# Kernel optimization log

Measured on AMD Instinct MI355X. Metric: run time of the kernel, lower is better.

The kernel has to match this reference:

```python
import jax, jax.numpy as jnp
import numpy as np

# ---- config (from init_kwargs) ----
BASE_SIZE = 16
RATIOS = np.array([0.5, 1.0, 2.0])
N_LAYERS = 3
SCALES = 2.0 ** np.arange(N_LAYERS)
STRIDE = 16
PRE_NMS_TOPN = 2000
POST_NMS_TOPN = 300
MIN_THRESHOLD = 16.0
NMS_THRESH = 0.7
IMG_W = 1024
IMG_H = 1024
B, H, W = 16, 64, 64
A = len(RATIOS) * len(SCALES)  # 9


def _whctrs(a):
    w = a[2] - a[0] + 1.0
    h = a[3] - a[1] + 1.0
    return w, h, a[0] + 0.5 * (w - 1.0), a[1] + 0.5 * (h - 1.0)


def _mkanchors(ws, hs, cx, cy):
    return np.stack([cx - 0.5 * (ws - 1.0), cy - 0.5 * (hs - 1.0),
                     cx + 0.5 * (ws - 1.0), cy + 0.5 * (hs - 1.0)], axis=1)


def _generate_anchors():
    base = np.array([0.0, 0.0, BASE_SIZE - 1.0, BASE_SIZE - 1.0])
    w, h, cx, cy = _whctrs(base)
    size = w * h
    ws = np.round(np.sqrt(size / RATIOS))
    hs = np.round(ws * RATIOS)
    ratio_anchors = _mkanchors(ws, hs, np.full_like(ws, cx), np.full_like(ws, cy))
    out = []
    for ra in ratio_anchors:
        rw, rh, rcx, rcy = _whctrs(ra)
        out.append(_mkanchors(rw * SCALES, rh * SCALES,
                              np.full_like(SCALES, rcx), np.full_like(SCALES, rcy)))
    return np.concatenate(out, axis=0)  # (A, 4)


def _all_anchors(height, width):
    anchors = _generate_anchors()  # (A, 4)
    sx = np.arange(width) * STRIDE
    sy = np.arange(height) * STRIDE
    sx, sy = np.meshgrid(sx, sy)  # (H, W) row-major over y -> matches permute(0,2,3,1)
    shifts = np.stack([sx.ravel(), sy.ravel(), sx.ravel(), sy.ravel()], axis=1)  # (K, 4)
    return (anchors[None, :, :] + shifts[:, None, :]).reshape(-1, 4).astype(np.float32)  # (K*A, 4)


def _decode(deltas, anchors):
    # bbox_reg_to_coord: standard bbox_transform_inv
    aw = anchors[:, 2] - anchors[:, 0] + 1.0
    ah = anchors[:, 3] - anchors[:, 1] + 1.0
    acx = anchors[:, 0] + 0.5 * aw
    acy = anchors[:, 1] + 0.5 * ah
    cx = deltas[..., 0] * aw + acx
    cy = deltas[..., 1] * ah + acy
    pw = jnp.exp(deltas[..., 2]) * aw
    ph = jnp.exp(deltas[..., 3]) * ah
    return jnp.stack([cx - 0.5 * pw, cy - 0.5 * ph,
                      cx + 0.5 * pw, cy + 0.5 * ph], axis=-1)


def _nms_single(boxes, scores):
    # boxes: (N, 4) sorted by descending score
    N = boxes.shape[0]
    x1, y1, x2, y2 = boxes[:, 0], boxes[:, 1], boxes[:, 2], boxes[:, 3]
    areas = (x2 - x1 + 1.0) * (y2 - y1 + 1.0)
    iw = jnp.maximum(0.0, jnp.minimum(x2[:, None], x2[None, :]) - jnp.maximum(x1[:, None], x1[None, :]) + 1.0)
    ih = jnp.maximum(0.0, jnp.minimum(y2[:, None], y2[None, :]) - jnp.maximum(y1[:, None], y1[None, :]) + 1.0)
    inter = iw * ih
    iou = inter / (areas[:, None] + areas[None, :] - inter)  # (N, N)
    idx = jnp.arange(N)

    def body(sup, i):  # greedy sequential NMS
        keep_i = ~sup[i]
        sup = sup | (keep_i & (iou[i] > NMS_THRESH) & (idx > i))
        return sup, keep_i

    _, keep = jax.lax.scan(body, jnp.zeros(N, dtype=bool), idx)
    # kept boxes first, preserving score order; fixed-size output padded with zeros
    prio = jnp.where(keep, idx, idx + N)
    order = jnp.argsort(prio)[:POST_NMS_TOPN]
    valid = keep[order]
    out_boxes = jnp.where(valid[:, None], boxes[order], 0.0)
    out_scores = jnp.where(valid, scores[order], 0.0)
    return out_boxes, out_scores


def reference(labels_pred, bbox_reg):
    b, _, h, w = labels_pred.shape
    anchors = jnp.asarray(_all_anchors(h, w))  # (K*A, 4)
    scores = labels_pred.transpose(0, 2, 3, 1).reshape(b, -1, 2)[..., 1]  # (B, K*A)
    deltas = bbox_reg.transpose(0, 2, 3, 1).reshape(b, -1, 4)  # (B, K*A, 4)
    boxes = _decode(deltas, anchors)
    boxes = jnp.stack([
        jnp.clip(boxes[..., 0], 0.0, IMG_W - 1.0),
        jnp.clip(boxes[..., 1], 0.0, IMG_H - 1.0),
        jnp.clip(boxes[..., 2], 0.0, IMG_W - 1.0),
        jnp.clip(boxes[..., 3], 0.0, IMG_H - 1.0)], axis=-1)
    keep = ((boxes[..., 2] - boxes[..., 0] + 1.0 >= MIN_THRESHOLD)
            & (boxes[..., 3] - boxes[..., 1] + 1.0 >= MIN_THRESHOLD))
    masked = jnp.where(keep, scores, -jnp.inf)
    top_scores, top_idx = jax.lax.top_k(masked, PRE_NMS_TOPN)  # (B, pre)
    top_boxes = jnp.take_along_axis(boxes, top_idx[..., None], axis=1)  # (B, pre, 4)
    return jax.vmap(_nms_single)(top_boxes, top_scores)


def setup_inputs() -> dict:
    key = jax.random.key(0)
    k1, k2 = jax.random.split(key)
    labels_pred = jax.random.normal(k1, (B, 2 * A, H, W), dtype=jnp.float32)
    bbox_reg = jax.random.normal(k2, (B, 4 * A, H, W), dtype=jnp.float32) * 0.2
    return {"labels_pred": labels_pred, "bbox_reg": bbox_reg}
```

## Files before the change

### kernel.cpp

```cpp
#include <hip/hip_runtime.h>
#include <stdint.h>

#pragma clang fp contract(off)

typedef unsigned long long ull;

#define NB 16
#define NA 9
#define HW 4096
#define NANCH (NA*HW)
#define TOTAL (NB*NANCH)
#define TOPN 2000
#define PADN 2048
#define SELPAD 3072
#define OUTN 300
#define HBITS 13
#define HBINS (1 << HBITS)
#define MNMS 384
#define MSTRIPS (MNMS/64)
#define MPITCH 8
#define GD2 16

#define MIDC 0x1.666667p-1

__constant__ float c_ax1[9] = {-3.5f,-15.f,-38.f,  0.f, -8.f,-24.f,  2.5f, -3.f,-14.f};
__constant__ float c_ay1[9] = { 2.f,  -4.f,-16.f,  0.f, -8.f,-24.f, -3.f,-14.f,-36.f};
__constant__ float c_ax2[9] = {18.5f, 30.f, 53.f, 15.f, 23.f, 39.f, 12.5f, 18.f, 29.f};
__constant__ float c_ay2[9] = {13.f,  19.f, 31.f, 15.f, 23.f, 39.f, 18.f,  29.f, 51.f};

__device__ __forceinline__ void decode_box(int a, int x, int y,
    float d0, float d1, float d2, float d3,
    float& x1, float& y1, float& x2, float& y2) {
  float ax1 = c_ax1[a] + 16.f * (float)x;
  float ay1 = c_ay1[a] + 16.f * (float)y;
  float ax2 = c_ax2[a] + 16.f * (float)x;
  float ay2 = c_ay2[a] + 16.f * (float)y;
  float aw  = ax2 - ax1 + 1.f;
  float ah  = ay2 - ay1 + 1.f;
  float acx = ax1 + 0.5f * aw;
  float acy = ay1 + 0.5f * ah;
  float cx = d0 * aw + acx;
  float cy = d1 * ah + acy;
  float pw = expf(d2) * aw;
  float ph = expf(d3) * ah;
  x1 = cx - 0.5f * pw;
  y1 = cy - 0.5f * ph;
  x2 = cx + 0.5f * pw;
  y2 = cy + 0.5f * ph;
  x1 = fminf(fmaxf(x1, 0.f), 1023.f);
  y1 = fminf(fmaxf(y1, 0.f), 1023.f);
  x2 = fminf(fmaxf(x2, 0.f), 1023.f);
  y2 = fminf(fmaxf(y2, 0.f), 1023.f);
}

__device__ __forceinline__ uint32_t f2ord(float f) {
  uint32_t u = __float_as_uint(f);
  return (u & 0x80000000u) ? ~u : (u | 0x80000000u);
}
__device__ __forceinline__ float ord2f(uint32_t u) {
  return (u & 0x80000000u) ? __uint_as_float(u ^ 0x80000000u) : __uint_as_float(~u);
}

__global__ void k_score(const float* __restrict__ labels, const float* __restrict__ bbox,
                        uint32_t* __restrict__ keys) {
  int t = blockIdx.x * 256 + threadIdx.x;
  if (t >= TOTAL) return;
  int pos = t & (HW - 1);
  int ba  = t >> 12;
  int a = ba % 9, b = ba / 9;
  float score = labels[((b * 18 + 2 * a + 1) << 12) + pos];
  const float* dp = bbox + ((b * 36 + 4 * a) << 12) + pos;
  float d0 = dp[0], d1 = dp[4096], d2 = dp[8192], d3 = dp[12288];
  int y = pos >> 6, x = pos & 63;
  float x1, y1, x2, y2;
  decode_box(a, x, y, d0, d1, d2, d3, x1, y1, x2, y2);
  bool keep = (x2 - x1 + 1.f >= 16.f) && (y2 - y1 + 1.f >= 16.f);
  float s = keep ? score : -INFINITY;
  keys[t] = f2ord(s);
}

__global__ __launch_bounds__(1024) void k_batch(const uint32_t* __restrict__ keys,
                                                ull* __restrict__ selKeys,
                                                uint32_t* __restrict__ counters) {
  int b = blockIdx.x, tid = threadIdx.x;
  int wave = tid >> 6, lane = tid & 63;
  __shared__ uint32_t hist[HBINS];
  __shared__ uint32_t wtot[16];
  __shared__ uint32_t sh_T, sh_cnt;
  const uint32_t* kb = keys + b * NANCH;
  const uint4* kb4 = (const uint4*)kb;
#pragma unroll
  for (int k = 0; k < HBINS / 1024; ++k) hist[k * 1024 + tid] = 0u;
  if (tid == 0) { sh_T = 0u; sh_cnt = 0u; }
  __syncthreads();
  for (int i4 = tid; i4 < NANCH / 4; i4 += 1024) {
    uint4 v = kb4[i4];
    if (v.x & 0x80000000u) atomicAdd(&hist[v.x >> (32 - HBITS)], 1u);
    if (v.y & 0x80000000u) atomicAdd(&hist[v.y >> (32 - HBITS)], 1u);
    if (v.z & 0x80000000u) atomicAdd(&hist[v.z >> (32 - HBITS)], 1u);
    if (v.w & 0x80000000u) atomicAdd(&hist[v.w >> (32 - HBITS)], 1u);
  }
  __syncthreads();
  uint32_t c[8], suf[8];
#pragma unroll
  for (int k = 0; k < 8; ++k) c[k] = hist[tid * 8 + k];
  suf[7] = c[7];
#pragma unroll
  for (int k = 6; k >= 0; --k) suf[k] = c[k] + suf[k + 1];
  uint32_t total = suf[0];
  uint32_t wsuf = total;
#pragma unroll
  for (int off = 1; off < 64; off <<= 1) {
    uint32_t v = __shfl_down(wsuf, off);
    if (lane + off < 64) wsuf += v;
  }
  if (lane == 0) wtot[wave] = wsuf;
  __syncthreads();
  uint32_t wab = 0;
  for (int w = wave + 1; w < 16; ++w) wab += wtot[w];
  uint32_t ssum = wsuf + wab;
  uint32_t above_t = ssum - total;
  if (above_t < TOPN && ssum >= TOPN) {
    uint32_t T = (uint32_t)(tid * 8);
#pragma unroll
    for (int k = 7; k >= 0; --k) {
      uint32_t ab = above_t + ((k < 7) ? suf[k + 1] : 0u);
      if (ab < TOPN && ab + c[k] >= TOPN) T = (uint32_t)(tid * 8 + k);
    }
    sh_T = T;
  }
  __syncthreads();
  uint32_t T = sh_T;
  for (int i4 = tid; i4 < NANCH / 4; i4 += 1024) {
    uint4 v = kb4[i4];
    uint32_t vv[4] = { v.x, v.y, v.z, v.w };
#pragma unroll
    for (int cc = 0; cc < 4; ++cc) {
      uint32_t u = vv[cc];
      if ((u >> (32 - HBITS)) >= T) {
        uint32_t slot = atomicAdd(&sh_cnt, 1u);
        if (slot < SELPAD) {
          int i = i4 * 4 + cc;
          uint32_t canon = (uint32_t)((i & 4095) * 9 + (i >> 12));
          selKeys[b * SELPAD + slot] = (((ull)(~u)) << 32) | canon;
        }
      }
    }
  }
  __syncthreads();
  if (tid == 0) counters[b] = (sh_cnt < SELPAD) ? sh_cnt : SELPAD;
}

__global__ __launch_bounds__(256) void k_rank(const ull* __restrict__ selKeys,
                        const uint32_t* __restrict__ counters, const float* __restrict__ bbox,
                        float4* __restrict__ boxes, float* __restrict__ areas,
                        float* __restrict__ selScore) {
  int b = blockIdx.y;
  int i = blockIdx.x * 256 + threadIdx.x;
  int tid = threadIdx.x;
  uint32_t n = counters[b];
  const ull* sk = selKeys + b * SELPAD;
  ull ki = (i < (int)n) ? sk[i] : ~0ull;
  int rank = 0;
  __shared__ ull chunk[256];
  for (uint32_t base = 0; base < n; base += 256) {
    uint32_t j = base + (uint32_t)tid;
    chunk[tid] = (j < n) ? sk[j] : ~0ull;
    __syncthreads();
    int lim = (int)(n - base < 256u ? n - base : 256u);
    for (int t2 = 0; t2 < lim; ++t2) rank += (chunk[t2] < ki) ? 1 : 0;
    __syncthreads();
  }
  if (i < (int)n && rank < TOPN) {
    uint32_t idx = (uint32_t)ki;
    selScore[b * TOPN + rank] = ord2f(~((uint32_t)(ki >> 32)));
    int pos = (int)idx / 9, a = (int)idx - 9 * pos;
    int y = pos >> 6, x = pos & 63;
    const float* dp = bbox + ((b * 36 + 4 * a) << 12) + pos;
    float d0 = dp[0], d1 = dp[4096], d2 = dp[8192], d3 = dp[12288];
    float x1, y1, x2, y2;
    decode_box(a, x, y, d0, d1, d2, d3, x1, y1, x2, y2);
    boxes[b * PADN + rank] = make_float4(x1, y1, x2, y2);
    areas[b * PADN + rank] = (x2 - x1 + 1.f) * (y2 - y1 + 1.f);
  }
}

__global__ __launch_bounds__(256) void k_mask(const float4* __restrict__ boxes,
                                              const float* __restrict__ areas,
                                              ull* __restrict__ gmask) {
  int rb = blockIdx.x, b = blockIdx.y;
  int tid = threadIdx.x, wv = tid >> 6, lane = tid & 63;
  int rbase = rb * 32;
  int smin = rbase >> 6;
  __shared__ float4 sRow[32];
  __shared__ float  sAr[32];
  if (tid < 32) {
    sRow[tid] = boxes[b * PADN + rbase + tid];
    sAr[tid]  = areas[b * PADN + rbase + tid];
  }
  float4 bj[MSTRIPS];
  float  ja[MSTRIPS];
#pragma unroll
  for (int s = 0; s < MSTRIPS; ++s) {
    if (s >= smin) {
      bj[s] = boxes[b * PADN + (s << 6) + lane];
      ja[s] = areas[b * PADN + (s << 6) + lane];
    }
  }
  __syncthreads();
  const double MD = MIDC;
  for (int r = wv; r < 32; r += 4) {
    int i = rbase + r;
    float4 bi = sRow[r];
    float  ia = sAr[r];
#pragma unroll
    for (int s = 0; s < MSTRIPS; ++s) {
      if (s < smin) continue;
      int j = (s << 6) + lane;
      float iw = fminf(bi.z, bj[s].z) - fmaxf(bi.x, bj[s].x) + 1.f; iw = fmaxf(iw, 0.f);
      float ih = fminf(bi.w, bj[s].w) - fmaxf(bi.y, bj[s].y) + 1.f; ih = fmaxf(ih, 0.f);
      float inter = iw * ih;
      float uu = (ia + ja[s]) - inter;
      bool sup = (j > i) && ((double)inter >= MD * (double)uu);
      ull mb = __ballot(sup);
      if (lane == 0) gmask[((size_t)b * MNMS + i) * MPITCH + s] = mb;
    }
  }
}

__global__ __launch_bounds__(64) void k_scan(const ull* __restrict__ gmask,
                                             const float4* __restrict__ boxes,
                                             const float* __restrict__ areas,
                                             const float* __restrict__ selScore,
                                             float* __restrict__ out) {
  int b = blockIdx.x, lane = threadIdx.x;
  const ull* mb = gmask + (size_t)b * MNMS * MPITCH;
  int l8 = lane & 7;
  __shared__ int kidx[OUTN];
  __shared__ int sh_cnt;
  const double MD = MIDC;
  ull supw = 0ull;
  int cnt = 0;
  ull pf[GD2];
#pragma unroll
  for (int ph = 0; ph < GD2; ++ph) pf[ph] = mb[ph * MPITCH + l8];
  for (int base = 0; base < MNMS && cnt < OUTN; base += GD2) {
#pragma unroll
    for (int ph = 0; ph < GD2; ++ph) {
      int i = base + ph;
      ull bal = __ballot(((supw >> (i & 63)) & 1ull) != 0ull);
      if (!((bal >> (i >> 6)) & 1ull)) {
        ull mm = (l8 >= (i >> 6) && l8 < MSTRIPS) ? pf[ph] : 0ull;
        supw |= mm;
        if (lane == 0 && cnt < OUTN) kidx[cnt] = i;
        cnt++;
      }
      int nx = i + GD2; if (nx > MNMS - 1) nx = MNMS - 1;
      pf[ph] = mb[nx * MPITCH + l8];
    }
  }
  for (int i = MNMS; i < TOPN && cnt < OUTN; ++i) {
    float4 bi = boxes[b * PADN + i];
    float ia = areas[b * PADN + i];
    bool sup = false;
    for (int cb = 0; cb < cnt; cb += 64) {
      int k = cb + lane;
      if (k < cnt) {
        int kj = kidx[k];
        float4 bk = boxes[b * PADN + kj];
        float ka = areas[b * PADN + kj];
        float iw = fminf(bi.z, bk.z) - fmaxf(bi.x, bk.x) + 1.f; iw = fmaxf(iw, 0.f);
        float ih = fminf(bi.w, bk.w) - fmaxf(bi.y, bk.y) + 1.f; ih = fmaxf(ih, 0.f);
        float inter = iw * ih;
        float uu = (ia + ka) - inter;
        sup = sup || ((double)inter >= MD * (double)uu);
      }
    }
    if (!__any(sup)) {
      if (lane == 0) kidx[cnt] = i;
      cnt++;
    }
  }
  if (lane == 0) sh_cnt = (cnt < OUTN) ? cnt : OUTN;
  __syncthreads();
  int c = sh_cnt;
  float4* ob = (float4*)out;
  for (int s2 = lane; s2 < OUTN; s2 += 64) {
    float4 bx = make_float4(0.f, 0.f, 0.f, 0.f);
    float sc = 0.f;
    if (s2 < c) {
      int i = kidx[s2];
      bx = boxes[b * PADN + i];
      sc = selScore[b * TOPN + i];
    }
    ob[b * OUTN + s2] = bx;
    out[NB * OUTN * 4 + b * OUTN + s2] = sc;
  }
}

extern "C" void kernel_launch(void* const* d_in, const int* in_sizes, int n_in,
                              void* d_out, int out_size, void* d_ws, size_t ws_size,
                              hipStream_t stream) {
  const float* labels = (const float*)d_in[0];
  const float* bbox   = (const float*)d_in[1];
  char* ws = (char*)d_ws;
  uint32_t* keys    = (uint32_t*)(ws + 0);
  ull* selKeys      = (ull*)(ws + 2359296);
  float* selScore   = (float*)(ws + 2752512);
  float* areas      = (float*)(ws + 2880512);
  float4* boxes     = (float4*)(ws + 3011584);
  uint32_t* counters= (uint32_t*)(ws + 3535872);
  ull* gmask        = (ull*)(ws + 3535936);
  float* out = (float*)d_out;

  hipLaunchKernelGGL(k_score, dim3((TOTAL + 255) / 256), dim3(256), 0, stream, labels, bbox, keys);
  hipLaunchKernelGGL(k_batch, dim3(NB), dim3(1024), 0, stream, keys, selKeys, counters);
  hipLaunchKernelGGL(k_rank,  dim3(SELPAD / 256, NB), dim3(256), 0, stream, selKeys, counters, bbox, boxes, areas, selScore);
  hipLaunchKernelGGL(k_mask,  dim3(MNMS / 32, NB), dim3(256), 0, stream, boxes, areas, gmask);
  hipLaunchKernelGGL(k_scan,  dim3(NB), dim3(64), 0, stream, gmask, boxes, areas, selScore, out);
}
```

Measured before the change: 90.42 us.

## Fuse rank, mask and scan kernels with per-batch atomic flags; vectorize scoring

Merges the rank, IoU-mask and greedy-scan kernels into one launch. Blocks are split by role, and later-stage blocks spin on per-batch global counters that the earlier-stage blocks increment after a threadfence. This removes two kernel launch gaps and lets batches proceed independently. It also vectorizes k_score to handle four anchors per thread with float4 loads and a uint4 store. The spin-wait relies on producer blocks being scheduled before or alongside consumers, which carries a deadlock risk if they are not. The done counters are reset inside k_score.

```diff
diff --git a/kernel.cpp b/kernel.cpp
--- a/kernel.cpp
+++ b/kernel.cpp
@@ -62,21 +62,35 @@
 }
 
 __global__ void k_score(const float* __restrict__ labels, const float* __restrict__ bbox,
-                        uint32_t* __restrict__ keys) {
-  int t = blockIdx.x * 256 + threadIdx.x;
-  if (t >= TOTAL) return;
-  int pos = t & (HW - 1);
-  int ba  = t >> 12;
+                        uint32_t* __restrict__ keys, uint32_t* __restrict__ done) {
+  int t4 = blockIdx.x * 256 + threadIdx.x;
+  if (blockIdx.x == 0) { done[threadIdx.x] = 0u; done[256 + threadIdx.x] = 0u; }
+  int p4 = t4 & 1023;
+  int pos = p4 << 2;
+  int ba = t4 >> 10;
   int a = ba % 9, b = ba / 9;
-  float score = labels[((b * 18 + 2 * a + 1) << 12) + pos];
-  const float* dp = bbox + ((b * 36 + 4 * a) << 12) + pos;
-  float d0 = dp[0], d1 = dp[4096], d2 = dp[8192], d3 = dp[12288];
-  int y = pos >> 6, x = pos & 63;
-  float x1, y1, x2, y2;
-  decode_box(a, x, y, d0, d1, d2, d3, x1, y1, x2, y2);
-  bool keep = (x2 - x1 + 1.f >= 16.f) && (y2 - y1 + 1.f >= 16.f);
-  float s = keep ? score : -INFINITY;
-  keys[t] = f2ord(s);
+  float4 sc  = ((const float4*)(labels + ((b * 18 + 2 * a + 1) << 12)))[p4];
+  const float* dpb = bbox + ((b * 36 + 4 * a) << 12);
+  float4 d0v = ((const float4*)(dpb        ))[p4];
+  float4 d1v = ((const float4*)(dpb +  4096))[p4];
+  float4 d2v = ((const float4*)(dpb +  8192))[p4];
+  float4 d3v = ((const float4*)(dpb + 12288))[p4];
+  int y = pos >> 6, x0 = pos & 63;
+  float scA[4] = { sc.x,  sc.y,  sc.z,  sc.w  };
+  float d0A[4] = { d0v.x, d0v.y, d0v.z, d0v.w };
+  float d1A[4] = { d1v.x, d1v.y, d1v.z, d1v.w };
+  float d2A[4] = { d2v.x, d2v.y, d2v.z, d2v.w };
+  float d3A[4] = { d3v.x, d3v.y, d3v.z, d3v.w };
+  uint32_t kout[4];
+#pragma unroll
+  for (int k = 0; k < 4; ++k) {
+    float x1, y1, x2, y2;
+    decode_box(a, x0 + k, y, d0A[k], d1A[k], d2A[k], d3A[k], x1, y1, x2, y2);
+    bool keep = (x2 - x1 + 1.f >= 16.f) && (y2 - y1 + 1.f >= 16.f);
+    kout[k] = f2ord(keep ? scA[k] : -INFINITY);
+  }
+  ((uint4*)(keys + b * NANCH + (a << 12) + pos))[0] =
+      make_uint4(kout[0], kout[1], kout[2], kout[3]);
 }
 
 __global__ __launch_bounds__(1024) void k_batch(const uint32_t* __restrict__ keys,
@@ -151,150 +165,162 @@
   if (tid == 0) counters[b] = (sh_cnt < SELPAD) ? sh_cnt : SELPAD;
 }
 
-__global__ __launch_bounds__(256) void k_rank(const ull* __restrict__ selKeys,
-                        const uint32_t* __restrict__ counters, const float* __restrict__ bbox,
-                        float4* __restrict__ boxes, float* __restrict__ areas,
-                        float* __restrict__ selScore) {
-  int b = blockIdx.y;
-  int i = blockIdx.x * 256 + threadIdx.x;
-  int tid = threadIdx.x;
-  uint32_t n = counters[b];
-  const ull* sk = selKeys + b * SELPAD;
-  ull ki = (i < (int)n) ? sk[i] : ~0ull;
-  int rank = 0;
-  __shared__ ull chunk[256];
-  for (uint32_t base = 0; base < n; base += 256) {
-    uint32_t j = base + (uint32_t)tid;
-    chunk[tid] = (j < n) ? sk[j] : ~0ull;
-    __syncthreads();
-    int lim = (int)(n - base < 256u ? n - base : 256u);
-    for (int t2 = 0; t2 < lim; ++t2) rank += (chunk[t2] < ki) ? 1 : 0;
-    __syncthreads();
-  }
-  if (i < (int)n && rank < TOPN) {
-    uint32_t idx = (uint32_t)ki;
-    selScore[b * TOPN + rank] = ord2f(~((uint32_t)(ki >> 32)));
-    int pos = (int)idx / 9, a = (int)idx - 9 * pos;
-    int y = pos >> 6, x = pos & 63;
-    const float* dp = bbox + ((b * 36 + 4 * a) << 12) + pos;
-    float d0 = dp[0], d1 = dp[4096], d2 = dp[8192], d3 = dp[12288];
-    float x1, y1, x2, y2;
-    decode_box(a, x, y, d0, d1, d2, d3, x1, y1, x2, y2);
-    boxes[b * PADN + rank] = make_float4(x1, y1, x2, y2);
-    areas[b * PADN + rank] = (x2 - x1 + 1.f) * (y2 - y1 + 1.f);
-  }
-}
-
-__global__ __launch_bounds__(256) void k_mask(const float4* __restrict__ boxes,
-                                              const float* __restrict__ areas,
-                                              ull* __restrict__ gmask) {
-  int rb = blockIdx.x, b = blockIdx.y;
-  int tid = threadIdx.x, wv = tid >> 6, lane = tid & 63;
-  int rbase = rb * 32;
-  int smin = rbase >> 6;
-  __shared__ float4 sRow[32];
-  __shared__ float  sAr[32];
-  if (tid < 32) {
-    sRow[tid] = boxes[b * PADN + rbase + tid];
-    sAr[tid]  = areas[b * PADN + rbase + tid];
-  }
-  float4 bj[MSTRIPS];
-  float  ja[MSTRIPS];
-#pragma unroll
-  for (int s = 0; s < MSTRIPS; ++s) {
-    if (s >= smin) {
-      bj[s] = boxes[b * PADN + (s << 6) + lane];
-      ja[s] = areas[b * PADN + (s << 6) + lane];
-    }
-  }
-  __syncthreads();
+__global__ __launch_bounds__(256) void k_post(
+    const ull* __restrict__ selKeys, const uint32_t* __restrict__ counters,
+    const float* __restrict__ bbox, float4* __restrict__ boxes,
+    float* __restrict__ areas, float* __restrict__ selScore,
+    ull* __restrict__ gmask, float* __restrict__ out, uint32_t* __restrict__ done) {
+  int unit = blockIdx.x, b = blockIdx.y, tid = threadIdx.x;
   const double MD = MIDC;
-  for (int r = wv; r < 32; r += 4) {
-    int i = rbase + r;
-    float4 bi = sRow[r];
-    float  ia = sAr[r];
+
+  if (unit < 12) {
+    int i = unit * 256 + tid;
+    uint32_t n = counters[b];
+    const ull* sk = selKeys + b * SELPAD;
+    ull ki = (i < (int)n) ? sk[i] : ~0ull;
+    int rank = 0;
+    __shared__ ull chunk[256];
+    for (uint32_t base = 0; base < n; base += 256) {
+      uint32_t j = base + (uint32_t)tid;
+      chunk[tid] = (j < n) ? sk[j] : ~0ull;
+      __syncthreads();
+      int lim = (int)(n - base < 256u ? n - base : 256u);
+      for (int t2 = 0; t2 < lim; ++t2) rank += (chunk[t2] < ki) ? 1 : 0;
+      __syncthreads();
+    }
+    if (i < (int)n && rank < TOPN) {
+      uint32_t idx = (uint32_t)ki;
+      selScore[b * TOPN + rank] = ord2f(~((uint32_t)(ki >> 32)));
+      int pos = (int)idx / 9, a = (int)idx - 9 * pos;
+      int y = pos >> 6, x = pos & 63;
+      const float* dp = bbox + ((b * 36 + 4 * a) << 12) + pos;
+      float d0 = dp[0], d1 = dp[4096], d2 = dp[8192], d3 = dp[12288];
+      float x1, y1, x2, y2;
+      decode_box(a, x, y, d0, d1, d2, d3, x1, y1, x2, y2);
+      boxes[b * PADN + rank] = make_float4(x1, y1, x2, y2);
+      areas[b * PADN + rank] = (x2 - x1 + 1.f) * (y2 - y1 + 1.f);
+    }
+    __threadfence();
+    __syncthreads();
+    if (tid == 0) atomicAdd(&done[b * 16], 1u);
+
+  } else if (unit < 24) {
+    if (tid == 0) {
+      while (atomicAdd(&done[b * 16], 0u) < 12u) __builtin_amdgcn_s_sleep(2);
+    }
+    __syncthreads();
+    __threadfence();
+    int rb = unit - 12;
+    int wv = tid >> 6, lane = tid & 63;
+    int rbase = rb * 32;
+    int smin = rbase >> 6;
+    __shared__ float4 sRow[32];
+    __shared__ float  sAr[32];
+    if (tid < 32) {
+      sRow[tid] = boxes[b * PADN + rbase + tid];
+      sAr[tid]  = areas[b * PADN + rbase + tid];
+    }
+    float4 bj[MSTRIPS];
+    float  ja[MSTRIPS];
 #pragma unroll
     for (int s = 0; s < MSTRIPS; ++s) {
-      if (s < smin) continue;
-      int j = (s << 6) + lane;
-      float iw = fminf(bi.z, bj[s].z) - fmaxf(bi.x, bj[s].x) + 1.f; iw = fmaxf(iw, 0.f);
-      float ih = fminf(bi.w, bj[s].w) - fmaxf(bi.y, bj[s].y) + 1.f; ih = fmaxf(ih, 0.f);
-      float inter = iw * ih;
-      float uu = (ia + ja[s]) - inter;
-      bool sup = (j > i) && ((double)inter >= MD * (double)uu);
-      ull mb = __ballot(sup);
-      if (lane == 0) gmask[((size_t)b * MNMS + i) * MPITCH + s] = mb;
-    }
-  }
-}
-
-__global__ __launch_bounds__(64) void k_scan(const ull* __restrict__ gmask,
-                                             const float4* __restrict__ boxes,
-                                             const float* __restrict__ areas,
-                                             const float* __restrict__ selScore,
-                                             float* __restrict__ out) {
-  int b = blockIdx.x, lane = threadIdx.x;
-  const ull* mb = gmask + (size_t)b * MNMS * MPITCH;
-  int l8 = lane & 7;
-  __shared__ int kidx[OUTN];
-  __shared__ int sh_cnt;
-  const double MD = MIDC;
-  ull supw = 0ull;
-  int cnt = 0;
-  ull pf[GD2];
-#pragma unroll
-  for (int ph = 0; ph < GD2; ++ph) pf[ph] = mb[ph * MPITCH + l8];
-  for (int base = 0; base < MNMS && cnt < OUTN; base += GD2) {
-#pragma unroll
-    for (int ph = 0; ph < GD2; ++ph) {
-      int i = base + ph;
-      ull bal = __ballot(((supw >> (i & 63)) & 1ull) != 0ull);
-      if (!((bal >> (i >> 6)) & 1ull)) {
-        ull mm = (l8 >= (i >> 6) && l8 < MSTRIPS) ? pf[ph] : 0ull;
-        supw |= mm;
-        if (lane == 0 && cnt < OUTN) kidx[cnt] = i;
-        cnt++;
-      }
-      int nx = i + GD2; if (nx > MNMS - 1) nx = MNMS - 1;
-      pf[ph] = mb[nx * MPITCH + l8];
-    }
-  }
-  for (int i = MNMS; i < TOPN && cnt < OUTN; ++i) {
-    float4 bi = boxes[b * PADN + i];
-    float ia = areas[b * PADN + i];
-    bool sup = false;
-    for (int cb = 0; cb < cnt; cb += 64) {
-      int k = cb + lane;
-      if (k < cnt) {
-        int kj = kidx[k];
-        float4 bk = boxes[b * PADN + kj];
-        float ka = areas[b * PADN + kj];
-        float iw = fminf(bi.z, bk.z) - fmaxf(bi.x, bk.x) + 1.f; iw = fmaxf(iw, 0.f);
-        float ih = fminf(bi.w, bk.w) - fmaxf(bi.y, bk.y) + 1.f; ih = fmaxf(ih, 0.f);
+      if (s >= smin) {
+        bj[s] = boxes[b * PADN + (s << 6) + lane];
+        ja[s] = areas[b * PADN + (s << 6) + lane];
+      }
+    }
+    __syncthreads();
+    for (int r = wv; r < 32; r += 4) {
+      int i = rbase + r;
+      float4 bi = sRow[r];
+      float  ia = sAr[r];
+#pragma unroll
+      for (int s = 0; s < MSTRIPS; ++s) {
+        if (s < smin) continue;
+        int j = (s << 6) + lane;
+        float iw = fminf(bi.z, bj[s].z) - fmaxf(bi.x, bj[s].x) + 1.f; iw = fmaxf(iw, 0.f);
+        float ih = fminf(bi.w, bj[s].w) - fmaxf(bi.y, bj[s].y) + 1.f; ih = fmaxf(ih, 0.f);
         float inter = iw * ih;
-        float uu = (ia + ka) - inter;
-        sup = sup || ((double)inter >= MD * (double)uu);
-      }
-    }
-    if (!__any(sup)) {
-      if (lane == 0) kidx[cnt] = i;
-      cnt++;
-    }
-  }
-  if (lane == 0) sh_cnt = (cnt < OUTN) ? cnt : OUTN;
-  __syncthreads();
-  int c = sh_cnt;
-  float4* ob = (float4*)out;
-  for (int s2 = lane; s2 < OUTN; s2 += 64) {
-    float4 bx = make_float4(0.f, 0.f, 0.f, 0.f);
-    float sc = 0.f;
-    if (s2 < c) {
-      int i = kidx[s2];
-      bx = boxes[b * PADN + i];
-      sc = selScore[b * TOPN + i];
-    }
-    ob[b * OUTN + s2] = bx;
-    out[NB * OUTN * 4 + b * OUTN + s2] = sc;
+        float uu = (ia + ja[s]) - inter;
+        bool sup = (j > i) && ((double)inter >= MD * (double)uu);
+        ull mb = __ballot(sup);
+        if (lane == 0) gmask[((size_t)b * MNMS + i) * MPITCH + s] = mb;
+      }
+    }
+    __threadfence();
+    __syncthreads();
+    if (tid == 0) atomicAdd(&done[256 + b * 16], 1u);
+
+  } else {
+    if (tid == 0) {
+      while (atomicAdd(&done[256 + b * 16], 0u) < 12u) __builtin_amdgcn_s_sleep(2);
+    }
+    __syncthreads();
+    __threadfence();
+    __shared__ int kidx[OUTN];
+    __shared__ int sh_cnt;
+    if (tid < 64) {
+      int lane = tid;
+      const ull* mb = gmask + (size_t)b * MNMS * MPITCH;
+      int l8 = lane & 7;
+      ull supw = 0ull;
+      int cnt = 0;
+      ull pf[GD2];
+#pragma unroll
+      for (int ph = 0; ph < GD2; ++ph) pf[ph] = mb[ph * MPITCH + l8];
+      for (int base = 0; base < MNMS && cnt < OUTN; base += GD2) {
+#pragma unroll
+        for (int ph = 0; ph < GD2; ++ph) {
+          int i = base + ph;
+          ull bal = __ballot(((supw >> (i & 63)) & 1ull) != 0ull);
+          if (!((bal >> (i >> 6)) & 1ull)) {
+            ull mm = (l8 >= (i >> 6) && l8 < MSTRIPS) ? pf[ph] : 0ull;
+            supw |= mm;
+            if (lane == 0 && cnt < OUTN) kidx[cnt] = i;
+            cnt++;
+          }
+          int nx = i + GD2; if (nx > MNMS - 1) nx = MNMS - 1;
+          pf[ph] = mb[nx * MPITCH + l8];
+        }
+      }
+      for (int i = MNMS; i < TOPN && cnt < OUTN; ++i) {
+        float4 bi = boxes[b * PADN + i];
+        float ia = areas[b * PADN + i];
+        bool sup = false;
+        for (int cb = 0; cb < cnt; cb += 64) {
+          int k = cb + lane;
+          if (k < cnt) {
+            int kj = kidx[k];
+            float4 bk = boxes[b * PADN + kj];
+            float ka = areas[b * PADN + kj];
+            float iw = fminf(bi.z, bk.z) - fmaxf(bi.x, bk.x) + 1.f; iw = fmaxf(iw, 0.f);
+            float ih = fminf(bi.w, bk.w) - fmaxf(bi.y, bk.y) + 1.f; ih = fmaxf(ih, 0.f);
+            float inter = iw * ih;
+            float uu = (ia + ka) - inter;
+            sup = sup || ((double)inter >= MD * (double)uu);
+          }
+        }
+        if (!__any(sup)) {
+          if (lane == 0) kidx[cnt] = i;
+          cnt++;
+        }
+      }
+      if (lane == 0) sh_cnt = (cnt < OUTN) ? cnt : OUTN;
+    }
+    __syncthreads();
+    int c = sh_cnt;
+    float4* ob = (float4*)out;
+    for (int s2 = tid; s2 < OUTN; s2 += 256) {
+      float4 bx = make_float4(0.f, 0.f, 0.f, 0.f);
+      float sc = 0.f;
+      if (s2 < c) {
+        int i = kidx[s2];
+        bx = boxes[b * PADN + i];
+        sc = selScore[b * TOPN + i];
+      }
+      ob[b * OUTN + s2] = bx;
+      out[NB * OUTN * 4 + b * OUTN + s2] = sc;
+    }
   }
 }
 
@@ -311,11 +337,11 @@
   float4* boxes     = (float4*)(ws + 3011584);
   uint32_t* counters= (uint32_t*)(ws + 3535872);
   ull* gmask        = (ull*)(ws + 3535936);
+  uint32_t* done    = (uint32_t*)(ws + 3929152);
   float* out = (float*)d_out;
 
-  hipLaunchKernelGGL(k_score, dim3((TOTAL + 255) / 256), dim3(256), 0, stream, labels, bbox, keys);
+  hipLaunchKernelGGL(k_score, dim3(TOTAL / 4 / 256), dim3(256), 0, stream, labels, bbox, keys, done);
   hipLaunchKernelGGL(k_batch, dim3(NB), dim3(1024), 0, stream, keys, selKeys, counters);
-  hipLaunchKernelGGL(k_rank,  dim3(SELPAD / 256, NB), dim3(256), 0, stream, selKeys, counters, bbox, boxes, areas, selScore);
-  hipLaunchKernelGGL(k_mask,  dim3(MNMS / 32, NB), dim3(256), 0, stream, boxes, areas, gmask);
-  hipLaunchKernelGGL(k_scan,  dim3(NB), dim3(64), 0, stream, gmask, boxes, areas, selScore, out);
-}
+  hipLaunchKernelGGL(k_post,  dim3(25, NB), dim3(256), 0, stream, selKeys, counters, bbox,
+                     boxes, areas, selScore, gmask, out, done);
+}
```

Result: slower. 140.9 us (+55.9%).

## Vectorize score kernel and rewrite NMS scan with LDS-staged masks and register bitsets

Applied to the files above, without the earlier changes.

The score kernel now has each thread handle four consecutive anchors, using float4 loads and a uint4 store to cut thread count and memory instructions. The NMS scan kernel first stages the per-batch suppression mask in LDS using 256 threads, zeroing strips that do not apply. A single wave then walks the rows with branchless bit operations that keep six suppression words in registers, uniformly across lanes instead of using per-row ballots. Kept indices are recovered afterwards by enumerating the bitset. This aims to cut the serial latency of the greedy scan, but it adds LDS staging and makes the wave recompute the same state redundantly in every lane.

```diff
diff --git a/kernel.cpp b/kernel.cpp
--- a/kernel.cpp
+++ b/kernel.cpp
@@ -19,7 +19,6 @@
 #define MNMS 384
 #define MSTRIPS (MNMS/64)
 #define MPITCH 8
-#define GD2 16
 
 #define MIDC 0x1.666667p-1
 
@@ -63,20 +62,33 @@
 
 __global__ void k_score(const float* __restrict__ labels, const float* __restrict__ bbox,
                         uint32_t* __restrict__ keys) {
-  int t = blockIdx.x * 256 + threadIdx.x;
-  if (t >= TOTAL) return;
-  int pos = t & (HW - 1);
-  int ba  = t >> 12;
+  int t4 = blockIdx.x * 256 + threadIdx.x;
+  int p4 = t4 & 1023;
+  int pos = p4 << 2;
+  int ba = t4 >> 10;
   int a = ba % 9, b = ba / 9;
-  float score = labels[((b * 18 + 2 * a + 1) << 12) + pos];
-  const float* dp = bbox + ((b * 36 + 4 * a) << 12) + pos;
-  float d0 = dp[0], d1 = dp[4096], d2 = dp[8192], d3 = dp[12288];
-  int y = pos >> 6, x = pos & 63;
-  float x1, y1, x2, y2;
-  decode_box(a, x, y, d0, d1, d2, d3, x1, y1, x2, y2);
-  bool keep = (x2 - x1 + 1.f >= 16.f) && (y2 - y1 + 1.f >= 16.f);
-  float s = keep ? score : -INFINITY;
-  keys[t] = f2ord(s);
+  float4 sc  = ((const float4*)(labels + ((b * 18 + 2 * a + 1) << 12)))[p4];
+  const float* dpb = bbox + ((b * 36 + 4 * a) << 12);
+  float4 d0v = ((const float4*)(dpb        ))[p4];
+  float4 d1v = ((const float4*)(dpb +  4096))[p4];
+  float4 d2v = ((const float4*)(dpb +  8192))[p4];
+  float4 d3v = ((const float4*)(dpb + 12288))[p4];
+  int y = pos >> 6, x0 = pos & 63;
+  float scA[4] = { sc.x,  sc.y,  sc.z,  sc.w  };
+  float d0A[4] = { d0v.x, d0v.y, d0v.z, d0v.w };
+  float d1A[4] = { d1v.x, d1v.y, d1v.z, d1v.w };
+  float d2A[4] = { d2v.x, d2v.y, d2v.z, d2v.w };
+  float d3A[4] = { d3v.x, d3v.y, d3v.z, d3v.w };
+  uint32_t kout[4];
+#pragma unroll
+  for (int k = 0; k < 4; ++k) {
+    float x1, y1, x2, y2;
+    decode_box(a, x0 + k, y, d0A[k], d1A[k], d2A[k], d3A[k], x1, y1, x2, y2);
+    bool keep = (x2 - x1 + 1.f >= 16.f) && (y2 - y1 + 1.f >= 16.f);
+    kout[k] = f2ord(keep ? scA[k] : -INFINITY);
+  }
+  ((uint4*)(keys + b * NANCH + (a << 12) + pos))[0] =
+      make_uint4(kout[0], kout[1], kout[2], kout[3]);
 }
 
 __global__ __launch_bounds__(1024) void k_batch(const uint32_t* __restrict__ keys,
@@ -228,67 +240,120 @@
   }
 }
 
-__global__ __launch_bounds__(64) void k_scan(const ull* __restrict__ gmask,
-                                             const float4* __restrict__ boxes,
-                                             const float* __restrict__ areas,
-                                             const float* __restrict__ selScore,
-                                             float* __restrict__ out) {
-  int b = blockIdx.x, lane = threadIdx.x;
-  const ull* mb = gmask + (size_t)b * MNMS * MPITCH;
-  int l8 = lane & 7;
+__global__ __launch_bounds__(256) void k_scan2(const ull* __restrict__ gmask,
+                                               const float4* __restrict__ boxes,
+                                               const float* __restrict__ areas,
+                                               const float* __restrict__ selScore,
+                                               float* __restrict__ out) {
+  int b = blockIdx.x, tid = threadIdx.x;
+  int lane = tid & 63;
+  __shared__ ull __attribute__((aligned(16))) lmr[MNMS][MPITCH];
   __shared__ int kidx[OUTN];
-  __shared__ int sh_cnt;
+  __shared__ int sh_c;
+  const ull* gm = gmask + (size_t)b * MNMS * MPITCH;
+  for (int k = tid; k < MNMS * MPITCH; k += 256) {
+    int row = k >> 3, w = k & 7;
+    bool valid = (w >= (row >> 6)) && (w < MSTRIPS);
+    ((ull*)lmr)[k] = valid ? gm[k] : 0ull;
+  }
+  __syncthreads();
   const double MD = MIDC;
-  ull supw = 0ull;
-  int cnt = 0;
-  ull pf[GD2];
-#pragma unroll
-  for (int ph = 0; ph < GD2; ++ph) pf[ph] = mb[ph * MPITCH + l8];
-  for (int base = 0; base < MNMS && cnt < OUTN; base += GD2) {
-#pragma unroll
-    for (int ph = 0; ph < GD2; ++ph) {
-      int i = base + ph;
-      ull bal = __ballot(((supw >> (i & 63)) & 1ull) != 0ull);
-      if (!((bal >> (i >> 6)) & 1ull)) {
-        ull mm = (l8 >= (i >> 6) && l8 < MSTRIPS) ? pf[ph] : 0ull;
-        supw |= mm;
-        if (lane == 0 && cnt < OUTN) kidx[cnt] = i;
-        cnt++;
+  if (tid < 64) {
+    ull sup0 = 0, sup1 = 0, sup2 = 0, sup3 = 0, sup4 = 0, sup5 = 0;
+    ull km0 = 0, km1 = 0, km2 = 0, km3 = 0, km4 = 0, km5 = 0;
+    int tot = 0;
+    bool fin = false;
+
+#define PR(W0, W1, W2, BITOFF, SUPC, KMC)                                   \
+    {                                                                        \
+      ull t = (SUPC >> (BITOFF)) & 1ull;                                     \
+      KMC |= (t ^ 1ull) << (BITOFF);                                         \
+      ull m = t - 1ull;                                                      \
+      sup0 |= (W0).x & m; sup1 |= (W0).y & m;                                \
+      sup2 |= (W1).x & m; sup3 |= (W1).y & m;                                \
+      sup4 |= (W2).x & m; sup5 |= (W2).y & m;                                \
+    }
+
+#define DO_CHUNK(C, SUPC, KMC)                                               \
+    if (!fin) {                                                              \
+      _Pragma("clang loop unroll(disable)")                                  \
+      for (int g = 0; g < 16; ++g) {                                         \
+        int i0 = ((C) << 6) + (g << 2);                                      \
+        const ulonglong2* rpa = (const ulonglong2*)lmr[i0];                  \
+        const ulonglong2* rpb = (const ulonglong2*)lmr[i0 + 1];              \
+        const ulonglong2* rpc = (const ulonglong2*)lmr[i0 + 2];              \
+        const ulonglong2* rpd = (const ulonglong2*)lmr[i0 + 3];              \
+        ulonglong2 a0 = rpa[0], a1 = rpa[1], a2 = rpa[2];                    \
+        ulonglong2 b0 = rpb[0], b1 = rpb[1], b2 = rpb[2];                    \
+        ulonglong2 c0 = rpc[0], c1 = rpc[1], c2 = rpc[2];                    \
+        ulonglong2 d0 = rpd[0], d1 = rpd[1], d2 = rpd[2];                    \
+        int bo = g << 2;                                                     \
+        PR(a0, a1, a2, bo,     SUPC, KMC);                                   \
+        PR(b0, b1, b2, bo + 1, SUPC, KMC);                                   \
+        PR(c0, c1, c2, bo + 2, SUPC, KMC);                                   \
+        PR(d0, d1, d2, bo + 3, SUPC, KMC);                                   \
+      }                                                                      \
+      tot += (int)__popcll(KMC);                                             \
+      if (tot >= OUTN) fin = true;                                           \
+    }
+
+    DO_CHUNK(0, sup0, km0);
+    DO_CHUNK(1, sup1, km1);
+    DO_CHUNK(2, sup2, km2);
+    DO_CHUNK(3, sup3, km3);
+    DO_CHUNK(4, sup4, km4);
+    DO_CHUNK(5, sup5, km5);
+#undef DO_CHUNK
+#undef PR
+
+    int cnt = 0;
+#define ENUM(KMC, C)                                                         \
+    {                                                                        \
+      ull w = KMC;                                                           \
+      while (w && cnt < OUTN) {                                              \
+        int k2 = (int)__builtin_ctzll(w);                                    \
+        w &= w - 1ull;                                                       \
+        if (lane == 0) kidx[cnt] = ((C) << 6) + k2;                          \
+        cnt++;                                                               \
+      }                                                                      \
+    }
+    ENUM(km0, 0); ENUM(km1, 1); ENUM(km2, 2);
+    ENUM(km3, 3); ENUM(km4, 4); ENUM(km5, 5);
+#undef ENUM
+
+    if (cnt < OUTN) {
+      for (int i = MNMS; i < TOPN && cnt < OUTN; ++i) {
+        float4 bi = boxes[b * PADN + i];
+        float ia = areas[b * PADN + i];
+        bool sup = false;
+        for (int cb2 = 0; cb2 < cnt; cb2 += 64) {
+          int k = cb2 + lane;
+          if (k < cnt) {
+            int kj = kidx[k];
+            float4 bk = boxes[b * PADN + kj];
+            float ka = areas[b * PADN + kj];
+            float iw = fminf(bi.z, bk.z) - fmaxf(bi.x, bk.x) + 1.f; iw = fmaxf(iw, 0.f);
+            float ih = fminf(bi.w, bk.w) - fmaxf(bi.y, bk.y) + 1.f; ih = fmaxf(ih, 0.f);
+            float inter = iw * ih;
+            float uu = (ia + ka) - inter;
+            sup = sup || ((double)inter >= MD * (double)uu);
+          }
+        }
+        if (!__any(sup)) {
+          if (lane == 0) kidx[cnt] = i;
+          cnt++;
+        }
       }
-      int nx = i + GD2; if (nx > MNMS - 1) nx = MNMS - 1;
-      pf[ph] = mb[nx * MPITCH + l8];
-    }
-  }
-  for (int i = MNMS; i < TOPN && cnt < OUTN; ++i) {
-    float4 bi = boxes[b * PADN + i];
-    float ia = areas[b * PADN + i];
-    bool sup = false;
-    for (int cb = 0; cb < cnt; cb += 64) {
-      int k = cb + lane;
-      if (k < cnt) {
-        int kj = kidx[k];
-        float4 bk = boxes[b * PADN + kj];
-        float ka = areas[b * PADN + kj];
-        float iw = fminf(bi.z, bk.z) - fmaxf(bi.x, bk.x) + 1.f; iw = fmaxf(iw, 0.f);
-        float ih = fminf(bi.w, bk.w) - fmaxf(bi.y, bk.y) + 1.f; ih = fmaxf(ih, 0.f);
-        float inter = iw * ih;
-        float uu = (ia + ka) - inter;
-        sup = sup || ((double)inter >= MD * (double)uu);
-      }
-    }
-    if (!__any(sup)) {
-      if (lane == 0) kidx[cnt] = i;
-      cnt++;
-    }
-  }
-  if (lane == 0) sh_cnt = (cnt < OUTN) ? cnt : OUTN;
-  __syncthreads();
-  int c = sh_cnt;
+    }
+    if (lane == 0) sh_c = (cnt < OUTN) ? cnt : OUTN;
+  }
+  __syncthreads();
+  int c2 = sh_c;
   float4* ob = (float4*)out;
-  for (int s2 = lane; s2 < OUTN; s2 += 64) {
+  for (int s2 = tid; s2 < OUTN; s2 += 256) {
     float4 bx = make_float4(0.f, 0.f, 0.f, 0.f);
     float sc = 0.f;
-    if (s2 < c) {
+    if (s2 < c2) {
       int i = kidx[s2];
       bx = boxes[b * PADN + i];
       sc = selScore[b * TOPN + i];
@@ -313,9 +378,9 @@
   ull* gmask        = (ull*)(ws + 3535936);
   float* out = (float*)d_out;
 
-  hipLaunchKernelGGL(k_score, dim3((TOTAL + 255) / 256), dim3(256), 0, stream, labels, bbox, keys);
+  hipLaunchKernelGGL(k_score, dim3(TOTAL / 4 / 256), dim3(256), 0, stream, labels, bbox, keys);
   hipLaunchKernelGGL(k_batch, dim3(NB), dim3(1024), 0, stream, keys, selKeys, counters);
   hipLaunchKernelGGL(k_rank,  dim3(SELPAD / 256, NB), dim3(256), 0, stream, selKeys, counters, bbox, boxes, areas, selScore);
   hipLaunchKernelGGL(k_mask,  dim3(MNMS / 32, NB), dim3(256), 0, stream, boxes, areas, gmask);
-  hipLaunchKernelGGL(k_scan,  dim3(NB), dim3(64), 0, stream, gmask, boxes, areas, selScore, out);
-}
+  hipLaunchKernelGGL(k_scan2, dim3(NB), dim3(256), 0, stream, gmask, boxes, areas, selScore, out);
+}
```

Result: slower. 107.2 us (+18.6%).

## Vectorize score kernel and enlarge bitmask NMS window to 768 candidates

Applied to the files above, without the earlier changes.

The score/filter kernel now handles four anchors per thread with float4 loads and one uint4 store, which cuts the number of memory instructions. The bitmask NMS window grows from 384 to 768 candidates, with a wider mask pitch and 16 lanes scanning strips. More boxes are therefore resolved by the fast ballot scan instead of the slow serial fallback loop. In exchange the mask kernel does four times the pairwise IoU work and the scan has twice as many rows to walk.

```diff
diff --git a/kernel.cpp b/kernel.cpp
--- a/kernel.cpp
+++ b/kernel.cpp
@@ -16,9 +16,9 @@
 #define OUTN 300
 #define HBITS 13
 #define HBINS (1 << HBITS)
-#define MNMS 384
+#define MNMS 768
 #define MSTRIPS (MNMS/64)
-#define MPITCH 8
+#define MPITCH 16
 #define GD2 16
 
 #define MIDC 0x1.666667p-1
@@ -63,20 +63,33 @@
 
 __global__ void k_score(const float* __restrict__ labels, const float* __restrict__ bbox,
                         uint32_t* __restrict__ keys) {
-  int t = blockIdx.x * 256 + threadIdx.x;
-  if (t >= TOTAL) return;
-  int pos = t & (HW - 1);
-  int ba  = t >> 12;
+  int t4 = blockIdx.x * 256 + threadIdx.x;
+  int p4 = t4 & 1023;
+  int pos = p4 << 2;
+  int ba = t4 >> 10;
   int a = ba % 9, b = ba / 9;
-  float score = labels[((b * 18 + 2 * a + 1) << 12) + pos];
-  const float* dp = bbox + ((b * 36 + 4 * a) << 12) + pos;
-  float d0 = dp[0], d1 = dp[4096], d2 = dp[8192], d3 = dp[12288];
-  int y = pos >> 6, x = pos & 63;
-  float x1, y1, x2, y2;
-  decode_box(a, x, y, d0, d1, d2, d3, x1, y1, x2, y2);
-  bool keep = (x2 - x1 + 1.f >= 16.f) && (y2 - y1 + 1.f >= 16.f);
-  float s = keep ? score : -INFINITY;
-  keys[t] = f2ord(s);
+  float4 sc  = ((const float4*)(labels + ((b * 18 + 2 * a + 1) << 12)))[p4];
+  const float* dpb = bbox + ((b * 36 + 4 * a) << 12);
+  float4 d0v = ((const float4*)(dpb        ))[p4];
+  float4 d1v = ((const float4*)(dpb +  4096))[p4];
+  float4 d2v = ((const float4*)(dpb +  8192))[p4];
+  float4 d3v = ((const float4*)(dpb + 12288))[p4];
+  int y = pos >> 6, x0 = pos & 63;
+  float scA[4] = { sc.x,  sc.y,  sc.z,  sc.w  };
+  float d0A[4] = { d0v.x, d0v.y, d0v.z, d0v.w };
+  float d1A[4] = { d1v.x, d1v.y, d1v.z, d1v.w };
+  float d2A[4] = { d2v.x, d2v.y, d2v.z, d2v.w };
+  float d3A[4] = { d3v.x, d3v.y, d3v.z, d3v.w };
+  uint32_t kout[4];
+#pragma unroll
+  for (int k = 0; k < 4; ++k) {
+    float x1, y1, x2, y2;
+    decode_box(a, x0 + k, y, d0A[k], d1A[k], d2A[k], d3A[k], x1, y1, x2, y2);
+    bool keep = (x2 - x1 + 1.f >= 16.f) && (y2 - y1 + 1.f >= 16.f);
+    kout[k] = f2ord(keep ? scA[k] : -INFINITY);
+  }
+  ((uint4*)(keys + b * NANCH + (a << 12) + pos))[0] =
+      make_uint4(kout[0], kout[1], kout[2], kout[3]);
 }
 
 __global__ __launch_bounds__(1024) void k_batch(const uint32_t* __restrict__ keys,
@@ -235,7 +248,7 @@
                                              float* __restrict__ out) {
   int b = blockIdx.x, lane = threadIdx.x;
   const ull* mb = gmask + (size_t)b * MNMS * MPITCH;
-  int l8 = lane & 7;
+  int l16 = lane & 15;
   __shared__ int kidx[OUTN];
   __shared__ int sh_cnt;
   const double MD = MIDC;
@@ -243,20 +256,20 @@
   int cnt = 0;
   ull pf[GD2];
 #pragma unroll
-  for (int ph = 0; ph < GD2; ++ph) pf[ph] = mb[ph * MPITCH + l8];
+  for (int ph = 0; ph < GD2; ++ph) pf[ph] = mb[ph * MPITCH + l16];
   for (int base = 0; base < MNMS && cnt < OUTN; base += GD2) {
 #pragma unroll
     for (int ph = 0; ph < GD2; ++ph) {
       int i = base + ph;
       ull bal = __ballot(((supw >> (i & 63)) & 1ull) != 0ull);
       if (!((bal >> (i >> 6)) & 1ull)) {
-        ull mm = (l8 >= (i >> 6) && l8 < MSTRIPS) ? pf[ph] : 0ull;
+        ull mm = (l16 >= (i >> 6) && l16 < MSTRIPS) ? pf[ph] : 0ull;
         supw |= mm;
         if (lane == 0 && cnt < OUTN) kidx[cnt] = i;
         cnt++;
       }
       int nx = i + GD2; if (nx > MNMS - 1) nx = MNMS - 1;
-      pf[ph] = mb[nx * MPITCH + l8];
+      pf[ph] = mb[nx * MPITCH + l16];
     }
   }
   for (int i = MNMS; i < TOPN && cnt < OUTN; ++i) {
@@ -313,7 +326,7 @@
   ull* gmask        = (ull*)(ws + 3535936);
   float* out = (float*)d_out;
 
-  hipLaunchKernelGGL(k_score, dim3((TOTAL + 255) / 256), dim3(256), 0, stream, labels, bbox, keys);
+  hipLaunchKernelGGL(k_score, dim3(TOTAL / 4 / 256), dim3(256), 0, stream, labels, bbox, keys);
   hipLaunchKernelGGL(k_batch, dim3(NB), dim3(1024), 0, stream, keys, selKeys, counters);
   hipLaunchKernelGGL(k_rank,  dim3(SELPAD / 256, NB), dim3(256), 0, stream, selKeys, counters, bbox, boxes, areas, selScore);
   hipLaunchKernelGGL(k_mask,  dim3(MNMS / 32, NB), dim3(256), 0, stream, boxes, areas, gmask);
```

Result: slower. 97.86 us (+8.2%).
